# Performance work log

Hardware: AMD Instinct MI355X
Metric: run time of the kernel (lower is better)

The kernel has to match this reference:

```python
import jax, jax.numpy as jnp
import numpy as np

LEVEL = 256
GROUPS = 1
SHIFT = (LEVEL - 1) / 2.0  # symmetric affine shift folded from quant.shift buffer


def qdq(x, clip_val, level=LEVEL, groups=GROUPS, shift=SHIFT):
    """Per-group clip + level quantize-dequantize (what custom_quant.Quant saves/restores).
    clip_val: [groups]. Group split is over equal contiguous chunks of the flattened tensor."""
    shp = x.shape
    xg = x.reshape(groups, -1)
    scale = (2.0 * clip_val) / (level - 1)          # [groups]
    scale = scale.reshape(groups, 1)
    q = jnp.clip(jnp.round(xg / scale + shift), 0.0, level - 1.0)
    return ((q - shift) * scale).reshape(shp)


def setup_inputs() -> dict:
    key = jax.random.key(0)
    k1, k2 = jax.random.split(key)
    # attention-style batched matmul: [B,H,S,Dh] @ [B,H,Dh,S]
    x1 = jax.random.normal(k1, (2, 12, 1024, 64), dtype=jnp.float32)
    x2 = jax.random.normal(k2, (2, 12, 64, 1024), dtype=jnp.float32)
    clip_val1 = 2.0 * jnp.ones((GROUPS,), dtype=jnp.float32)
    clip_val2 = 2.0 * jnp.ones((GROUPS,), dtype=jnp.float32)
    return {"x1": x1, "x2": x2, "clip_val1": clip_val1, "clip_val2": clip_val2}


def reference(x1, x2, clip_val1, clip_val2):
    # Faithful to matmul.forward: the quantized copies are only SAVED for backward;
    # the forward output itself is computed on the full-precision operands.
    # (qdq is exercised in the fwdbwd reference.)
    return jnp.matmul(x1, x2)  # [2,12,1024,1024]
```

## Files before the change

### kernel.cpp

```cpp
#include <hip/hip_runtime.h>
#include <hip/hip_bf16.h>


#define MM 1024
#define NN 1024
#define KK 64

typedef __attribute__((ext_vector_type(4))) float  float4v;
typedef __attribute__((ext_vector_type(4))) short  short4v;
typedef __attribute__((ext_vector_type(8))) short  bf16x8;
typedef __attribute__((ext_vector_type(16))) float floatx16;

__device__ __forceinline__ short f2bs(float f) {
    union { float f; unsigned u; } in;
    in.f = f;
    unsigned u = in.u;
    unsigned r = (u + 0x7FFFu + ((u >> 16) & 1u)) >> 16;
    return (short)r;
}

__global__ __launch_bounds__(256) void bmm_bf16_kernel(const float* __restrict__ A,
                                                       const float* __restrict__ B,
                                                       float* __restrict__ C) {
    __shared__ __align__(16) short a_sh[16 * 512];
    __shared__ __align__(16) short b_sh[16 * 512];

    const int tid = threadIdx.x;
    const int bx = blockIdx.x;
    const int by = blockIdx.y;
    const int bh = blockIdx.z;

    const int m0 = by * 128;
    const int n0 = bx * 128;

    const float* Ab = A + (size_t)bh * (MM * KK) + (size_t)m0 * KK;
    const float* Bb = B + (size_t)bh * (KK * NN) + n0;

    {
        const float4v* A4 = (const float4v*)Ab;
        #pragma unroll
        for (int i = 0; i < 8; ++i) {
            int f4 = tid + i * 256;
            float4v v = A4[f4];
            int m  = f4 >> 4;
            int k  = (f4 & 15) << 2;
            int mt = m >> 5;
            int ks = k >> 4;
            int q  = (k >> 3) & 1;
            int j0 = k & 7;
            int lane = (m & 31) + (q << 5);
            int dst = ((mt * 4 + ks) * 64 + lane) * 8 + j0;
            short4v s;
            s.x = f2bs(v.x); s.y = f2bs(v.y); s.z = f2bs(v.z); s.w = f2bs(v.w);
            *(short4v*)&a_sh[dst] = s;
        }
    }

    {
        int n  = tid & 127;
        int kh = tid >> 7;
        int nt = n >> 5;
        int lanebase = n & 31;
        #pragma unroll
        for (int s = 0; s < 8; ++s) {
            int k0 = kh * 4 + s * 8;
            float v0 = Bb[(size_t)(k0 + 0) * NN + n];
            float v1 = Bb[(size_t)(k0 + 1) * NN + n];
            float v2 = Bb[(size_t)(k0 + 2) * NN + n];
            float v3 = Bb[(size_t)(k0 + 3) * NN + n];
            int ks = k0 >> 4;
            int q  = (k0 >> 3) & 1;
            int j0 = k0 & 7;
            int lane = lanebase + (q << 5);
            int dst = ((nt * 4 + ks) * 64 + lane) * 8 + j0;
            short4v sv;
            sv.x = f2bs(v0); sv.y = f2bs(v1); sv.z = f2bs(v2); sv.w = f2bs(v3);
            *(short4v*)&b_sh[dst] = sv;
        }
    }

    __syncthreads();

    const int w    = tid >> 6;
    const int lane = tid & 63;
    const int wm   = (w >> 1) * 2;
    const int wn   = (w & 1) * 2;

    floatx16 acc[2][2];
    #pragma unroll
    for (int mi = 0; mi < 2; ++mi)
        #pragma unroll
        for (int ni = 0; ni < 2; ++ni)
            #pragma unroll
            for (int r = 0; r < 16; ++r)
                acc[mi][ni][r] = 0.0f;

    #pragma unroll
    for (int ks = 0; ks < 4; ++ks) {
        bf16x8 a0 = *(const bf16x8*)&a_sh[((wm + 0) * 4 + ks) * 512 + lane * 8];
        bf16x8 a1 = *(const bf16x8*)&a_sh[((wm + 1) * 4 + ks) * 512 + lane * 8];
        bf16x8 b0 = *(const bf16x8*)&b_sh[((wn + 0) * 4 + ks) * 512 + lane * 8];
        bf16x8 b1 = *(const bf16x8*)&b_sh[((wn + 1) * 4 + ks) * 512 + lane * 8];
        acc[0][0] = __builtin_amdgcn_mfma_f32_32x32x16_bf16(a0, b0, acc[0][0], 0, 0, 0);
        acc[0][1] = __builtin_amdgcn_mfma_f32_32x32x16_bf16(a0, b1, acc[0][1], 0, 0, 0);
        acc[1][0] = __builtin_amdgcn_mfma_f32_32x32x16_bf16(a1, b0, acc[1][0], 0, 0, 0);
        acc[1][1] = __builtin_amdgcn_mfma_f32_32x32x16_bf16(a1, b1, acc[1][1], 0, 0, 0);
    }

    float* Cb = C + (size_t)bh * (MM * NN) + (size_t)m0 * NN + n0;
    const int cc    = lane & 31;
    const int rbase = (lane >> 5) * 4;

    #pragma unroll
    for (int mi = 0; mi < 2; ++mi) {
        #pragma unroll
        for (int ni = 0; ni < 2; ++ni) {
            float* Ct = Cb + (size_t)((wm + mi) * 32) * NN + (wn + ni) * 32 + cc;
            #pragma unroll
            for (int r = 0; r < 16; ++r) {
                int row = rbase + (r & 3) + ((r >> 2) * 8);
                Ct[(size_t)row * NN] = acc[mi][ni][r];
            }
        }
    }
}

extern "C" void kernel_launch(void* const* d_in, const int* in_sizes, int n_in,
                              void* d_out, int out_size, void* d_ws, size_t ws_size,
                              hipStream_t stream) {
    const float* x1 = (const float*)d_in[0];
    const float* x2 = (const float*)d_in[1];
    float* out = (float*)d_out;

    dim3 grid(8, 8, 24);
    dim3 block(256);
    hipLaunchKernelGGL(bmm_bf16_kernel, grid, block, 0, stream, x1, x2, out);
}
```

Before: 125.3 us.

## Pre-convert operands to bf16 MFMA fragment layout in separate reformat kernels

Splits the kernel into two reformat passes that convert A and B to bf16 once, stored in workspace in MFMA-fragment order, plus a matmul kernel that loads fragments straight from global memory without shared memory or a barrier. It also swaps the MFMA operand order so each lane holds four consecutive output columns, which allows float4 vectorised stores instead of scalar strided stores. This removes the repeated fp32 loads and conversions done by every block that shares a row or column tile. The cost is two extra launches and a workspace round trip.

```diff
diff --git a/kernel.cpp b/kernel.cpp
--- a/kernel.cpp
+++ b/kernel.cpp
@@ -2,12 +2,10 @@
 #include <hip/hip_bf16.h>
 
 
-#define MM 1024
 #define NN 1024
 #define KK 64
 
 typedef __attribute__((ext_vector_type(4))) float  float4v;
-typedef __attribute__((ext_vector_type(4))) short  short4v;
 typedef __attribute__((ext_vector_type(8))) short  bf16x8;
 typedef __attribute__((ext_vector_type(16))) float floatx16;
 
@@ -15,76 +13,72 @@
     union { float f; unsigned u; } in;
     in.f = f;
     unsigned u = in.u;
-    unsigned r = (u + 0x7FFFu + ((u >> 16) & 1u)) >> 16;
-    return (short)r;
+    return (short)((u + 0x7FFFu + ((u >> 16) & 1u)) >> 16);
 }
 
-__global__ __launch_bounds__(256) void bmm_bf16_kernel(const float* __restrict__ A,
-                                                       const float* __restrict__ B,
-                                                       float* __restrict__ C) {
-    __shared__ __align__(16) short a_sh[16 * 512];
-    __shared__ __align__(16) short b_sh[16 * 512];
 
-    const int tid = threadIdx.x;
+__global__ __launch_bounds__(256) void reformat_A(const float* __restrict__ A,
+                                                  short* __restrict__ Aw) {
+    int t0 = blockIdx.x * 256 + threadIdx.x;
+    #pragma unroll
+    for (int it = 0; it < 4; ++it) {
+        int task = t0 + it * 49152;
+        int bh   = task >> 13;
+        int rem  = task & 8191;
+        int m    = rem >> 3;
+        int kg   = rem & 7;
+        const float4v* p = (const float4v*)(A + (size_t)task * 8);
+        float4v v0 = p[0];
+        float4v v1 = p[1];
+        int ks = kg >> 1, q = kg & 1;
+        int mt = m >> 5;
+        int lane = (m & 31) + (q << 5);
+        size_t dst = ((size_t)((bh * 32 + mt) * 4 + ks)) * 512 + (size_t)lane * 8;
+        bf16x8 o;
+        o[0] = f2bs(v0.x); o[1] = f2bs(v0.y); o[2] = f2bs(v0.z); o[3] = f2bs(v0.w);
+        o[4] = f2bs(v1.x); o[5] = f2bs(v1.y); o[6] = f2bs(v1.z); o[7] = f2bs(v1.w);
+        *(bf16x8*)(Aw + dst) = o;
+    }
+}
+
+__global__ __launch_bounds__(256) void reformat_B(const float* __restrict__ B,
+                                                  short* __restrict__ Bw) {
+    int t0 = blockIdx.x * 256 + threadIdx.x;
+    #pragma unroll
+    for (int it = 0; it < 4; ++it) {
+        int task = t0 + it * 49152;
+        int kg   = task / 24576;
+        int rem  = task - kg * 24576;
+        int bh   = rem >> 10;
+        int n    = rem & 1023;
+        const float* p = B + (size_t)bh * 65536 + (size_t)kg * 8192 + n;
+        float v0 = p[0 * 1024], v1 = p[1 * 1024], v2 = p[2 * 1024], v3 = p[3 * 1024];
+        float v4 = p[4 * 1024], v5 = p[5 * 1024], v6 = p[6 * 1024], v7 = p[7 * 1024];
+        int ks = kg >> 1, q = kg & 1;
+        int nt = n >> 5;
+        int lane = (n & 31) + (q << 5);
+        size_t dst = ((size_t)((bh * 32 + nt) * 4 + ks)) * 512 + (size_t)lane * 8;
+        bf16x8 o;
+        o[0] = f2bs(v0); o[1] = f2bs(v1); o[2] = f2bs(v2); o[3] = f2bs(v3);
+        o[4] = f2bs(v4); o[5] = f2bs(v5); o[6] = f2bs(v6); o[7] = f2bs(v7);
+        *(bf16x8*)(Bw + dst) = o;
+    }
+}
+
+__global__ __launch_bounds__(256) void bmm_frag(const short* __restrict__ Aw,
+                                                const short* __restrict__ Bw,
+                                                float* __restrict__ C) {
+    const int tid  = threadIdx.x;
+    const int lane = tid & 63;
+    const int w    = tid >> 6;
     const int bx = blockIdx.x;
     const int by = blockIdx.y;
     const int bh = blockIdx.z;
+    const int wm = (w >> 1) * 2;
+    const int wn = (w & 1) * 2;
 
-    const int m0 = by * 128;
-    const int n0 = bx * 128;
-
-    const float* Ab = A + (size_t)bh * (MM * KK) + (size_t)m0 * KK;
-    const float* Bb = B + (size_t)bh * (KK * NN) + n0;
-
-    {
-        const float4v* A4 = (const float4v*)Ab;
-        #pragma unroll
-        for (int i = 0; i < 8; ++i) {
-            int f4 = tid + i * 256;
-            float4v v = A4[f4];
-            int m  = f4 >> 4;
-            int k  = (f4 & 15) << 2;
-            int mt = m >> 5;
-            int ks = k >> 4;
-            int q  = (k >> 3) & 1;
-            int j0 = k & 7;
-            int lane = (m & 31) + (q << 5);
-            int dst = ((mt * 4 + ks) * 64 + lane) * 8 + j0;
-            short4v s;
-            s.x = f2bs(v.x); s.y = f2bs(v.y); s.z = f2bs(v.z); s.w = f2bs(v.w);
-            *(short4v*)&a_sh[dst] = s;
-        }
-    }
-
-    {
-        int n  = tid & 127;
-        int kh = tid >> 7;
-        int nt = n >> 5;
-        int lanebase = n & 31;
-        #pragma unroll
-        for (int s = 0; s < 8; ++s) {
-            int k0 = kh * 4 + s * 8;
-            float v0 = Bb[(size_t)(k0 + 0) * NN + n];
-            float v1 = Bb[(size_t)(k0 + 1) * NN + n];
-            float v2 = Bb[(size_t)(k0 + 2) * NN + n];
-            float v3 = Bb[(size_t)(k0 + 3) * NN + n];
-            int ks = k0 >> 4;
-            int q  = (k0 >> 3) & 1;
-            int j0 = k0 & 7;
-            int lane = lanebase + (q << 5);
-            int dst = ((nt * 4 + ks) * 64 + lane) * 8 + j0;
-            short4v sv;
-            sv.x = f2bs(v0); sv.y = f2bs(v1); sv.z = f2bs(v2); sv.w = f2bs(v3);
-            *(short4v*)&b_sh[dst] = sv;
-        }
-    }
-
-    __syncthreads();
-
-    const int w    = tid >> 6;
-    const int lane = tid & 63;
-    const int wm   = (w >> 1) * 2;
-    const int wn   = (w & 1) * 2;
+    const short* Ab = Aw + ((size_t)((bh * 32 + by * 4 + wm) * 4)) * 512 + (size_t)lane * 8;
+    const short* Bb = Bw + ((size_t)((bh * 32 + bx * 4 + wn) * 4)) * 512 + (size_t)lane * 8;
 
     floatx16 acc[2][2];
     #pragma unroll
@@ -97,29 +91,35 @@
 
     #pragma unroll
     for (int ks = 0; ks < 4; ++ks) {
-        bf16x8 a0 = *(const bf16x8*)&a_sh[((wm + 0) * 4 + ks) * 512 + lane * 8];
-        bf16x8 a1 = *(const bf16x8*)&a_sh[((wm + 1) * 4 + ks) * 512 + lane * 8];
-        bf16x8 b0 = *(const bf16x8*)&b_sh[((wn + 0) * 4 + ks) * 512 + lane * 8];
-        bf16x8 b1 = *(const bf16x8*)&b_sh[((wn + 1) * 4 + ks) * 512 + lane * 8];
-        acc[0][0] = __builtin_amdgcn_mfma_f32_32x32x16_bf16(a0, b0, acc[0][0], 0, 0, 0);
-        acc[0][1] = __builtin_amdgcn_mfma_f32_32x32x16_bf16(a0, b1, acc[0][1], 0, 0, 0);
-        acc[1][0] = __builtin_amdgcn_mfma_f32_32x32x16_bf16(a1, b0, acc[1][0], 0, 0, 0);
-        acc[1][1] = __builtin_amdgcn_mfma_f32_32x32x16_bf16(a1, b1, acc[1][1], 0, 0, 0);
+        bf16x8 a0 = *(const bf16x8*)(Ab + ks * 512);
+        bf16x8 a1 = *(const bf16x8*)(Ab + 2048 + ks * 512);
+        bf16x8 b0 = *(const bf16x8*)(Bb + ks * 512);
+        bf16x8 b1 = *(const bf16x8*)(Bb + 2048 + ks * 512);
+        acc[0][0] = __builtin_amdgcn_mfma_f32_32x32x16_bf16(b0, a0, acc[0][0], 0, 0, 0);
+        acc[0][1] = __builtin_amdgcn_mfma_f32_32x32x16_bf16(b1, a0, acc[0][1], 0, 0, 0);
+        acc[1][0] = __builtin_amdgcn_mfma_f32_32x32x16_bf16(b0, a1, acc[1][0], 0, 0, 0);
+        acc[1][1] = __builtin_amdgcn_mfma_f32_32x32x16_bf16(b1, a1, acc[1][1], 0, 0, 0);
     }
 
-    float* Cb = C + (size_t)bh * (MM * NN) + (size_t)m0 * NN + n0;
-    const int cc    = lane & 31;
-    const int rbase = (lane >> 5) * 4;
+    const int mc = lane & 31;
+    const int nb = (lane >> 5) * 4;
+    float* Cb = C + ((size_t)bh << 20)
+                  + (size_t)(by * 128 + wm * 32 + mc) * NN
+                  + bx * 128 + wn * 32 + nb;
 
     #pragma unroll
     for (int mi = 0; mi < 2; ++mi) {
         #pragma unroll
         for (int ni = 0; ni < 2; ++ni) {
-            float* Ct = Cb + (size_t)((wm + mi) * 32) * NN + (wn + ni) * 32 + cc;
+            float* Ct = Cb + (size_t)(mi * 32) * NN + ni * 32;
             #pragma unroll
-            for (int r = 0; r < 16; ++r) {
-                int row = rbase + (r & 3) + ((r >> 2) * 8);
-                Ct[(size_t)row * NN] = acc[mi][ni][r];
+            for (int g = 0; g < 4; ++g) {
+                float4v o;
+                o.x = acc[mi][ni][4 * g + 0];
+                o.y = acc[mi][ni][4 * g + 1];
+                o.z = acc[mi][ni][4 * g + 2];
+                o.w = acc[mi][ni][4 * g + 3];
+                *(float4v*)(Ct + 8 * g) = o;
             }
         }
     }
@@ -132,7 +132,10 @@
     const float* x2 = (const float*)d_in[1];
     float* out = (float*)d_out;
 
-    dim3 grid(8, 8, 24);
-    dim3 block(256);
-    hipLaunchKernelGGL(bmm_bf16_kernel, grid, block, 0, stream, x1, x2, out);
+    short* Aw = (short*)d_ws;
+    short* Bw = Aw + 1572864;
+
+    hipLaunchKernelGGL(reformat_A, dim3(192), dim3(256), 0, stream, x1, Aw);
+    hipLaunchKernelGGL(reformat_B, dim3(192), dim3(256), 0, stream, x2, Bw);
+    hipLaunchKernelGGL(bmm_frag, dim3(8, 8, 24), dim3(256), 0, stream, Aw, Bw, out);
 }
```

New measurement: 127.8 us. About the same (+2.0%).
